# Optimization experiments

Measured on AMD Instinct MI355X. Metric: run time of the kernel, lower is better.

Reference implementation:

```python
import jax, jax.numpy as jnp
import numpy as np

B, S, D = 1, 2048, 2048
H, KVH, HD = 32, 8, 64
FFN = 8192
N_EXPERTS, TOP_K = 32, 4
EPS = 1e-5
NEG = -1e9


def setup_inputs() -> dict:
    key = jax.random.key(0)
    ks = jax.random.split(key, 24)
    s = 0.02
    inp = {}
    inp['hidden_states'] = jax.random.normal(ks[0], (B, S, D), jnp.float32)
    # RoPE tables: cos/sin of shape [B, S, HD]
    inv_freq = 1.0 / (10000.0 ** (np.arange(0, HD, 2, dtype=np.float32) / HD))
    t = np.arange(S, dtype=np.float32)
    freqs = np.outer(t, inv_freq)                      # [S, HD/2]
    emb = np.concatenate([freqs, freqs], axis=-1)      # [S, HD]
    inp['cos'] = jnp.asarray(np.cos(emb))[None].repeat(B, axis=0)
    inp['sin'] = jnp.asarray(np.sin(emb))[None].repeat(B, axis=0)
    # additive causal mask [B, 1, S, S]
    causal = jnp.where(jnp.tril(jnp.ones((S, S), bool)), 0.0, NEG).astype(jnp.float32)
    inp['attention_mask'] = jnp.broadcast_to(causal[None, None], (B, 1, S, S))
    # attention params
    inp['wq'] = jax.random.normal(ks[1], (H * HD, D), jnp.float32) * s
    inp['bq'] = jnp.zeros((H * HD,), jnp.float32)
    inp['wk'] = jax.random.normal(ks[2], (KVH * HD, D), jnp.float32) * s
    inp['bk'] = jnp.zeros((KVH * HD,), jnp.float32)
    inp['wv'] = jax.random.normal(ks[3], (KVH * HD, D), jnp.float32) * s
    inp['bv'] = jnp.zeros((KVH * HD,), jnp.float32)
    inp['wo'] = jax.random.normal(ks[4], (D, H * HD), jnp.float32) * s
    inp['bo'] = jnp.zeros((D,), jnp.float32)
    # norms
    inp['ln1_w'] = jnp.ones((D,), jnp.float32)
    inp['ln2_w'] = jnp.ones((D,), jnp.float32)
    # MoE gate + shared expert MLP
    inp['gate_w'] = jax.random.normal(ks[5], (N_EXPERTS, D), jnp.float32) * s
    inp['gate_b'] = jnp.zeros((N_EXPERTS,), jnp.float32)
    inp['w1'] = jax.random.normal(ks[6], (FFN, D), jnp.float32) * s
    inp['b1'] = jnp.zeros((FFN,), jnp.float32)
    inp['w2'] = jax.random.normal(ks[7], (D, FFN), jnp.float32) * s
    inp['b2'] = jnp.zeros((D,), jnp.float32)
    inp['w3'] = jax.random.normal(ks[8], (FFN, D), jnp.float32) * s
    inp['b3'] = jnp.zeros((FFN,), jnp.float32)
    return inp


def _rms_norm(x, w, eps=EPS):
    x32 = x.astype(jnp.float32)
    var = jnp.mean(x32 * x32, axis=-1, keepdims=True)
    return (w * (x32 * jax.lax.rsqrt(var + eps))).astype(x.dtype)


def _rotate_half(x):
    x1, x2 = jnp.split(x, 2, axis=-1)
    return jnp.concatenate([-x2, x1], axis=-1)


def _decoder_layer(hidden_states, cos, sin, attention_mask,
                   wq, bq, wk, bk, wv, bv, wo, bo, ln1_w, ln2_w,
                   gate_w, gate_b, w1, b1, w2, b2, w3, b3):
    residual = hidden_states
    x = _rms_norm(hidden_states, ln1_w)

    # projections -> [B, heads, S, HD]
    q = (x @ wq.T + bq).reshape(B, S, H, HD).transpose(0, 2, 1, 3)
    k = (x @ wk.T + bk).reshape(B, S, KVH, HD).transpose(0, 2, 1, 3)
    v = (x @ wv.T + bv).reshape(B, S, KVH, HD).transpose(0, 2, 1, 3)

    # RoPE (cos/sin unsqueezed on head dim)
    c, s_ = cos[:, None], sin[:, None]
    q = q * c + _rotate_half(q) * s_
    k = k * c + _rotate_half(k) * s_

    # GQA: repeat kv heads
    n_rep = H // KVH
    k = jnp.repeat(k, n_rep, axis=1)
    v = jnp.repeat(v, n_rep, axis=1)

    scaling = HD ** -0.5
    scores = jnp.einsum('bhqd,bhkd->bhqk', q, k) * scaling + attention_mask
    probs = jax.nn.softmax(scores.astype(jnp.float32), axis=-1).astype(q.dtype)
    attn = jnp.einsum('bhqk,bhkd->bhqd', probs, v)
    attn = attn.transpose(0, 2, 1, 3).reshape(B, S, H * HD)
    attn = attn @ wo.T + bo

    hidden_states = residual + attn
    residual = hidden_states
    x = _rms_norm(hidden_states, ln2_w)

    # MoE block (as written in source: router computed, but ALL tokens go
    # through one shared expert MLP; routing weights unused in output)
    flat = x.reshape(-1, D)
    router_logits = flat @ gate_w.T + gate_b                     # [B*S, E]
    rw = jax.nn.softmax(router_logits.astype(jnp.float32), axis=-1)
    rw_top, sel = jax.lax.top_k(rw, TOP_K)                       # computed, unused
    del rw_top, sel

    h1 = flat @ w1.T + b1
    h3 = flat @ w3.T + b3
    mlp = (jax.nn.silu(h1) * h3) @ w2.T + b2
    hidden_states = residual + mlp.reshape(B, S, D)
    return hidden_states


def reference(hidden_states, cos, sin, attention_mask,
              wq, bq, wk, bk, wv, bv, wo, bo, ln1_w, ln2_w,
              gate_w, gate_b, w1, b1, w2, b2, w3, b3):
    return _decoder_layer(hidden_states, cos, sin, attention_mask,
                          wq, bq, wk, bk, wv, bv, wo, bo, ln1_w, ln2_w,
                          gate_w, gate_b, w1, b1, w2, b2, w3, b3)
```

## Files before the change

kernel.cpp:

```cpp
#include <hip/hip_runtime.h>

#define S_LEN 2048
#define DMODEL 2048
#define NH 32
#define NKV 8
#define HD 64
#define FFN_DIM 8192

typedef __attribute__((ext_vector_type(4))) float f32x4;
typedef __attribute__((ext_vector_type(4))) unsigned u32x4;
typedef __attribute__((ext_vector_type(16))) float f32x16;
typedef __attribute__((ext_vector_type(8))) short bf16x8;

#define MFMA(a, b, c) __builtin_amdgcn_mfma_f32_16x16x32_bf16(a, b, c, 0, 0, 0)
#define MFMA32(a, b, c) __builtin_amdgcn_mfma_f32_32x32x16_bf16(a, b, c, 0, 0, 0)

__device__ __forceinline__ ushort f2bf(float f) {
  unsigned u = __float_as_uint(f);
  unsigned r = (u + 0x7fffu + ((u >> 16) & 1u)) >> 16;
  return (ushort)r;
}
__device__ __forceinline__ float bf2f(ushort s) {
  return __uint_as_float(((unsigned)s) << 16);
}
__device__ __forceinline__ unsigned cvtpk(float a, float b) {
  unsigned r;
  asm("v_cvt_pk_bf16_f32 %0, %1, %2" : "=v"(r) : "v"(a), "v"(b));
  return r;
}

__device__ __forceinline__ void gload16(const void* g, void* l) {
  __builtin_amdgcn_global_load_lds(
      (const __attribute__((address_space(1))) void*)g,
      (__attribute__((address_space(3))) void*)l, 16, 0, 0);
}

__device__ __forceinline__ bf16x8 dsr128(const ushort* p) {
  unsigned addr =
      (unsigned)(size_t)(const __attribute__((address_space(3))) ushort*)p;
  u32x4 r;
  asm volatile("ds_read_b128 %0, %1" : "=&v"(r) : "v"(addr));
  return __builtin_bit_cast(bf16x8, r);
}

__global__ __launch_bounds__(256) void cvt_k(const float* __restrict__ in,
                                             ushort* __restrict__ out) {
  int i = blockIdx.x * 256 + threadIdx.x;
  f32x4 a = ((const f32x4*)in)[i * 2];
  f32x4 b = ((const f32x4*)in)[i * 2 + 1];
  bf16x8 r;
#pragma unroll
  for (int j = 0; j < 4; j++) r[j] = (short)f2bf(a[j]);
#pragma unroll
  for (int j = 0; j < 4; j++) r[4 + j] = (short)f2bf(b[j]);
  ((bf16x8*)out)[i] = r;
}

__global__ __launch_bounds__(256) void cvt_qkv_k(const float* __restrict__ wq,
                                                 const float* __restrict__ wk,
                                                 const float* __restrict__ wv,
                                                 ushort* __restrict__ dst) {
  int row = blockIdx.x;
  const float* src;
  if (row < 2048) src = wq + (size_t)row * DMODEL;
  else if (row < 2560) src = wk + (size_t)(row - 2048) * DMODEL;
  else src = wv + (size_t)(row - 2560) * DMODEL;
  int i = threadIdx.x * 8;
  f32x4 a = *(const f32x4*)(src + i);
  f32x4 b = *(const f32x4*)(src + i + 4);
  bf16x8 r;
#pragma unroll
  for (int j = 0; j < 4; j++) r[j] = (short)f2bf(a[j]);
#pragma unroll
  for (int j = 0; j < 4; j++) r[4 + j] = (short)f2bf(b[j]);
  *(bf16x8*)(dst + (size_t)row * DMODEL + i) = r;
}

__global__ __launch_bounds__(256) void bias3_k(const float* __restrict__ a,
                                               const float* __restrict__ b,
                                               const float* __restrict__ c,
                                               float* __restrict__ out) {
  int i = blockIdx.x * 256 + threadIdx.x;
  float v;
  if (i < 2048) v = a[i];
  else if (i < 2560) v = b[i - 2048];
  else v = c[i - 2560];
  out[i] = v;
}

__global__ __launch_bounds__(256) void rmsnorm_k(const float* __restrict__ in,
                                                 const float* __restrict__ w,
                                                 ushort* __restrict__ out) {
  const int row = blockIdx.x;
  const int tid = threadIdx.x;
  const float* x = in + (size_t)row * DMODEL;
  f32x4 v0 = *(const f32x4*)(x + tid * 8);
  f32x4 v1 = *(const f32x4*)(x + tid * 8 + 4);
  float ss = v0[0] * v0[0] + v0[1] * v0[1] + v0[2] * v0[2] + v0[3] * v0[3] +
             v1[0] * v1[0] + v1[1] * v1[1] + v1[2] * v1[2] + v1[3] * v1[3];
#pragma unroll
  for (int off = 32; off; off >>= 1) ss += __shfl_xor(ss, off, 64);
  __shared__ float red[4];
  if ((tid & 63) == 0) red[tid >> 6] = ss;
  __syncthreads();
  float tot = red[0] + red[1] + red[2] + red[3];
  float inv = rsqrtf(tot * (1.f / DMODEL) + 1e-5f);
#pragma unroll
  for (int i = 0; i < 8; i++) {
    int c = tid * 8 + i;
    float val = (i < 4) ? v0[i] : v1[i - 4];
    out[(size_t)row * DMODEL + c] = f2bf(w[c] * val * inv);
  }
}

__global__ __launch_bounds__(256) void rope_k(ushort* __restrict__ qkv,
                                              const float* __restrict__ cs,
                                              const float* __restrict__ sn) {
  int idx = blockIdx.x * 256 + threadIdx.x;
  int d = idx & 31;
  int t = idx >> 5;
  int head = t % (NH + NKV);
  int s = t / (NH + NKV);
  int col = (head < NH) ? head * HD : DMODEL + (head - NH) * HD;
  ushort* p = qkv + (size_t)s * 3072 + col;
  float lo = bf2f(p[d]), hi = bf2f(p[d + 32]);
  float c = cs[s * HD + d], si = sn[s * HD + d];
  p[d] = f2bf(lo * c - hi * si);
  p[d + 32] = f2bf(hi * c + lo * si);
}

enum { EPI_BF16 = 0, EPI_RESID = 1, EPI_SILU = 2, EPI_MUL = 3, EPI_PART = 4 };

#define QUAD(AS, BS, MROW, NCOL)                                     \
  _Pragma("unroll") for (int kk_ = 0; kk_ < 2; kk_++)                \
  _Pragma("unroll") for (int mf_ = 0; mf_ < 4; mf_++)                \
  _Pragma("unroll") for (int nf_ = 0; nf_ < 2; nf_++)                \
      acc[(MROW) + mf_][(NCOL) + nf_] =                              \
          MFMA(AS[2 * mf_ + kk_], BS[2 * nf_ + kk_],                 \
               acc[(MROW) + mf_][(NCOL) + nf_]);

#define PHASE_MID                                    \
  __builtin_amdgcn_sched_barrier(0);                 \
  __builtin_amdgcn_s_barrier();                      \
  asm volatile("s_waitcnt lgkmcnt(0)" ::: "memory"); \
  __builtin_amdgcn_sched_barrier(0);                 \
  __builtin_amdgcn_s_setprio(1);

#define PHASE_CLOSE                                  \
  __builtin_amdgcn_s_setprio(0);                     \
  __builtin_amdgcn_sched_barrier(0);                 \
  __builtin_amdgcn_s_barrier();

#define RD_A(PA0, PA1, J0)                           \
  _Pragma("unroll") for (int j_ = 0; j_ < 4; j_++) { \
    A_[2 * j_] = dsr128((PA0) + ((J0) + j_) * 1024); \
    A_[2 * j_ + 1] = dsr128((PA1) + ((J0) + j_) * 1024); \
  }
#define RD_B(DST, PB0, PB1, J0)                      \
  _Pragma("unroll") for (int n_ = 0; n_ < 2; n_++) { \
    DST[2 * n_] = dsr128((PB0) + ((J0) + n_) * 1024);\
    DST[2 * n_ + 1] = dsr128((PB1) + ((J0) + n_) * 1024); \
  }

template <int EPI>
__global__ __launch_bounds__(512, 2) void gemm256(
    const ushort* __restrict__ A, int lda, const ushort* __restrict__ B,
    int ldb, const float* __restrict__ bias, const float* __restrict__ resid,
    ushort* __restrict__ outb, float* __restrict__ outf, int ldc, int K,
    int kspan, long long opart) {
  __shared__ __align__(16) ushort lds[65536];
  const int tid = threadIdx.x;
  const int l = tid & 63, w = tid >> 6;
  const int g = l >> 4, r16 = l & 15;
  const int wm = w >> 2, wn = w & 3;

  int nwg = gridDim.x * gridDim.y;
  int bid = blockIdx.y * gridDim.x + blockIdx.x;
  bid = (bid & 7) * (nwg >> 3) + (bid >> 3);
  const int m0 = (bid % gridDim.x) * 256;
  const int n0 = (bid / gridDim.x) * 256;
  const int z = blockIdx.z;

  const ushort* Ag = A + (size_t)z * kspan + (size_t)m0 * lda;
  const ushort* Bg = B + (size_t)z * kspan + (size_t)n0 * ldb;
  ushort* outbz = outb;
  if (EPI == EPI_PART) outbz = outb + (size_t)z * opart;

  const int NT = K >> 6, NI = NT >> 1;

  const int stgRow = w * 8 + (l >> 3);
  const int stgCol = ((l & 7) ^ (l >> 3)) * 8;

  const int xa = (r16 & 7) << 4;
  const int c0 = ((g * 16) ^ xa) >> 1;
  const int c1 = c0 ^ 32;
  const int aslot = wm ? 24576 : 8192;
  const int bslot = ((wn >> 1) ? 16384 : 0) + (wn & 1) * 4096;
  const ushort* pA0b0 = lds + aslot + r16 * 64 + c0;
  const ushort* pA1b0 = lds + aslot + r16 * 64 + c1;
  const ushort* pA0b1 = pA0b0 + 32768;
  const ushort* pA1b1 = pA1b0 + 32768;
  const ushort* pB0b0 = lds + bslot + r16 * 64 + c0;
  const ushort* pB1b0 = lds + bslot + r16 * 64 + c1;
  const ushort* pB0b1 = pB0b0 + 32768;
  const ushort* pB1b1 = pB1b0 + 32768;

  f32x4 acc[8][4];
#pragma unroll
  for (int i = 0; i < 8; i++)
#pragma unroll
    for (int j = 0; j < 4; j++) acc[i][j] = (f32x4){0, 0, 0, 0};

  auto stageA = [&](int slot, int tile, int hf) {
    ushort* dst = lds + ((tile & 1) * 32768 + slot * 8192 + w * 512);
    const ushort* src =
        Ag + (size_t)(hf * 128 + stgRow) * lda + tile * 64 + stgCol;
    gload16(src, dst);
    gload16(src + (size_t)64 * lda, dst + 4096);
  };
  auto stageB = [&](int slot, int tile, int hf) {
    ushort* dst = lds + ((tile & 1) * 32768 + slot * 8192 + w * 512);
    const ushort* src =
        Bg + (size_t)(hf * 128 + stgRow) * ldb + tile * 64 + stgCol;
    gload16(src, dst);
    gload16(src + (size_t)64 * ldb, dst + 4096);
  };

  stageB(0, 0, 0);
  stageB(2, 0, 1);
  stageA(1, 0, 0);
  stageA(3, 0, 1);
  stageB(0, 1, 0);
  stageB(2, 1, 1);
  asm volatile("s_waitcnt vmcnt(4)" ::: "memory");
  __builtin_amdgcn_s_barrier();

  bf16x8 A_[8], Blo[4], Bhi[4];

  for (int i = 0; i < NI; ++i) {
    const int ta = 2 * i, tb = 2 * i + 1;
    const bool st = (ta + 2 < NT);
    RD_A(pA0b0, pA1b0, 0);
    RD_B(Blo, pB0b0, pB1b0, 0);
    stageA(1, tb, 0);
    asm volatile("s_waitcnt lgkmcnt(8)" ::: "memory");
    PHASE_MID; QUAD(A_, Blo, 0, 0); PHASE_CLOSE;
    RD_B(Bhi, pB0b0, pB1b0, 2);
    stageA(3, tb, 1);
    PHASE_MID; QUAD(A_, Bhi, 0, 2); PHASE_CLOSE;
    RD_A(pA0b0, pA1b0, 4);
    if (st) stageB(0, ta + 2, 0);
    PHASE_MID; QUAD(A_, Bhi, 4, 2); PHASE_CLOSE;
    if (st) stageB(2, ta + 2, 1);
    PHASE_MID; QUAD(A_, Blo, 4, 0);
    __builtin_amdgcn_s_setprio(0);
    __builtin_amdgcn_sched_barrier(0);
    if (st) {
      asm volatile("s_waitcnt vmcnt(4)" ::: "memory");
    } else {
      asm volatile("s_waitcnt vmcnt(0)" ::: "memory");
    }
    __builtin_amdgcn_s_barrier();
    RD_A(pA0b1, pA1b1, 0);
    RD_B(Blo, pB0b1, pB1b1, 0);
    if (st) stageA(1, ta + 2, 0);
    asm volatile("s_waitcnt lgkmcnt(8)" ::: "memory");
    PHASE_MID; QUAD(A_, Blo, 0, 0); PHASE_CLOSE;
    RD_B(Bhi, pB0b1, pB1b1, 2);
    if (st) stageA(3, ta + 2, 1);
    PHASE_MID; QUAD(A_, Bhi, 0, 2); PHASE_CLOSE;
    RD_A(pA0b1, pA1b1, 4);
    if (st) stageB(0, tb + 2, 0);
    PHASE_MID; QUAD(A_, Bhi, 4, 2); PHASE_CLOSE;
    if (st) stageB(2, tb + 2, 1);
    PHASE_MID; QUAD(A_, Blo, 4, 0);
    __builtin_amdgcn_s_setprio(0);
    __builtin_amdgcn_sched_barrier(0);
    asm volatile("s_waitcnt vmcnt(4)" ::: "memory");
    __builtin_amdgcn_s_barrier();
  }

#pragma unroll
  for (int mf = 0; mf < 8; mf++) {
#pragma unroll
    for (int nf = 0; nf < 4; nf++) {
      const int n = n0 + wn * 64 + nf * 16 + r16;
      float bia = (EPI == EPI_PART) ? 0.f : bias[n];
#pragma unroll
      for (int reg = 0; reg < 4; reg++) {
        const int m = m0 + wm * 128 + mf * 16 + g * 4 + reg;
        float v = acc[mf][nf][reg] + bia;
        if constexpr (EPI == EPI_BF16) {
          outbz[(size_t)m * ldc + n] = f2bf(v);
        } else if constexpr (EPI == EPI_RESID) {
          outf[(size_t)m * ldc + n] = v + resid[(size_t)m * ldc + n];
        } else if constexpr (EPI == EPI_SILU) {
          float sv = v / (1.f + __expf(-v));
          outbz[(size_t)m * ldc + n] = f2bf(sv);
        } else if constexpr (EPI == EPI_MUL) {
          float hv = bf2f(outbz[(size_t)m * ldc + n]);
          outbz[(size_t)m * ldc + n] = f2bf(v * hv);
        } else {
          outbz[(size_t)m * ldc + n] = f2bf(v);
        }
      }
    }
  }
}

template <int MODE>
__global__ __launch_bounds__(256) void reduce2_k(
    const ushort* __restrict__ part, long long pstride, int nz,
    const float* __restrict__ bias, int ncol, const float* __restrict__ resid,
    float* __restrict__ outf, ushort* __restrict__ outb) {
  long long i = (long long)(blockIdx.x * 256 + threadIdx.x) * 8;
  int col = (int)(i % ncol);
  float s[8];
#pragma unroll
  for (int j = 0; j < 8; j++) s[j] = bias[col + j];
  for (int zz = 0; zz < nz; zz++) {
    bf16x8 v = *(const bf16x8*)(part + zz * pstride + i);
#pragma unroll
    for (int j = 0; j < 8; j++) s[j] += bf2f((ushort)v[j]);
  }
  if constexpr (MODE == 1) {
#pragma unroll
    for (int j = 0; j < 8; j++) outf[i + j] = s[j] + resid[i + j];
  } else {
    bf16x8 r;
#pragma unroll
    for (int j = 0; j < 8; j++) r[j] = (short)f2bf(s[j]);
    *(bf16x8*)(outb + i) = r;
  }
}

__global__ __launch_bounds__(256, 3) void flash2_k(const ushort* __restrict__ qkv,
                                                   ushort* __restrict__ att) {
  const int bid = blockIdx.x;
  const int head = (bid >> 4) & 31;
  const int rmap = bid & 15;
  const int qb = (bid & 256) ? (15 - rmap) : rmap;
  const int kvh = head >> 2;
  const int tid = threadIdx.x;
  const int w = tid >> 6, l = tid & 63;
  const int h = l >> 5, q31 = l & 31;
  const int qw = qb * 128 + w * 32;
  const int qrow = qw + q31;

  __shared__ __align__(16) ushort lds[2][8192];

  bf16x8 qreg[4];
  {
    const ushort* qp = qkv + (size_t)qrow * 3072 + head * HD;
#pragma unroll
    for (int s = 0; s < 4; s++)
      qreg[s] = *(const bf16x8*)(qp + s * 16 + h * 8);
  }

  f32x16 oacc[2];
#pragma unroll
  for (int i = 0; i < 16; i++) { oacc[0][i] = 0.f; oacc[1][i] = 0.f; }
  float mreg = -1e30f, lsum = 0.f;

  const int nt = 2 * qb + 2;

  const int skv = tid >> 2;
  const int sch = (tid & 3) * 2;
  const int vkv = tid & 63;
  const int vd0 = (tid >> 6) * 16;

  const ushort* kg_base = qkv + DMODEL + kvh * HD;

  bf16x8 krA, krB, vrA, vrB;
  auto loadTile = [&](int jb) {
    const ushort* kg = kg_base + (size_t)jb * 64 * 3072;
    krA = *(const bf16x8*)(kg + (size_t)skv * 3072 + sch * 8);
    krB = *(const bf16x8*)(kg + (size_t)skv * 3072 + sch * 8 + 8);
    const ushort* vg = kg + 512;
    vrA = *(const bf16x8*)(vg + (size_t)vkv * 3072 + vd0);
    vrB = *(const bf16x8*)(vg + (size_t)vkv * 3072 + vd0 + 8);
  };
  auto writeTile = [&](int b) {
    ushort* kb = lds[b];
    *(bf16x8*)(kb + skv * 64 + ((sch ^ (skv & 7)) * 8)) = krA;
    *(bf16x8*)(kb + skv * 64 + (((sch + 1) ^ (skv & 7)) * 8)) = krB;
    ushort* vb = lds[b] + 4096;
#pragma unroll
    for (int i = 0; i < 8; i++) {
      int d = vd0 + i;
      vb[d * 64 + (((vkv >> 3) ^ (d & 7)) * 8) + (vkv & 7)] = (ushort)vrA[i];
    }
#pragma unroll
    for (int i = 0; i < 8; i++) {
      int d = vd0 + 8 + i;
      vb[d * 64 + (((vkv >> 3) ^ (d & 7)) * 8) + (vkv & 7)] = (ushort)vrB[i];
    }
  };

  loadTile(0);
  for (int jb = 0; jb < nt; ++jb) {
    const int b = jb & 1;
    writeTile(b);
    __syncthreads();
    if (jb + 1 < nt) loadTile(jb + 1);

    if (jb * 64 <= qw + 31) {
      const ushort* Kb = lds[b];
      const ushort* Vb = lds[b] + 4096;

      f32x16 sacc[2];
#pragma unroll
      for (int i = 0; i < 16; i++) { sacc[0][i] = 0.f; sacc[1][i] = 0.f; }
#pragma unroll
      for (int c = 0; c < 2; c++) {
        const int kvr = c * 32 + q31;
        const ushort* kp = Kb + kvr * 64;
        const int kx = kvr & 7;
#pragma unroll
        for (int s = 0; s < 4; s++) {
          bf16x8 kf = *(const bf16x8*)(kp + ((2 * s + h) ^ kx) * 8);
          sacc[c] = MFMA32(kf, qreg[s], sacc[c]);
        }
      }

      const bool diag = (jb * 64 + 63 > qw);
      if (diag) {
#pragma unroll
        for (int c = 0; c < 2; c++)
#pragma unroll
          for (int rg = 0; rg < 16; rg++) {
            int kvg = jb * 64 + c * 32 + (rg & 3) + 8 * (rg >> 2) + 4 * h;
            if (kvg > qrow) sacc[c][rg] = -1e30f;
          }
      }
      float tmax = sacc[0][0];
#pragma unroll
      for (int rg = 1; rg < 16; rg++) tmax = fmaxf(tmax, sacc[0][rg]);
#pragma unroll
      for (int rg = 0; rg < 16; rg++) tmax = fmaxf(tmax, sacc[1][rg]);
      tmax = fmaxf(tmax, __shfl_xor(tmax, 32));
      const float mn = fmaxf(mreg, tmax);
      const float resc = __expf((mreg - mn) * 0.125f);
      mreg = mn;
      float rsum = 0.f;
#pragma unroll
      for (int c = 0; c < 2; c++)
#pragma unroll
        for (int rg = 0; rg < 16; rg++) {
          float pv = __expf((sacc[c][rg] - mn) * 0.125f);
          sacc[c][rg] = pv;
          rsum += pv;
        }
      rsum += __shfl_xor(rsum, 32);
      lsum = lsum * resc + rsum;
      oacc[0] *= resc;
      oacc[1] *= resc;

      unsigned pw_[2][4][2];
#pragma unroll
      for (int c = 0; c < 2; c++)
#pragma unroll
        for (int rr = 0; rr < 4; rr++) {
          pw_[c][rr][0] = cvtpk(sacc[c][4 * rr + 0], sacc[c][4 * rr + 1]);
          pw_[c][rr][1] = cvtpk(sacc[c][4 * rr + 2], sacc[c][4 * rr + 3]);
        }

#pragma unroll
      for (int s = 0; s < 4; s++) {
        const int c = s >> 1, base = (s & 1) * 2;
        unsigned k0 = h ? pw_[c][base + 1][0] : pw_[c][base][0];
        unsigned k1 = h ? pw_[c][base + 1][1] : pw_[c][base][1];
        unsigned s0 = h ? pw_[c][base][0] : pw_[c][base + 1][0];
        unsigned s1 = h ? pw_[c][base][1] : pw_[c][base + 1][1];
        unsigned t0 = __shfl_xor(s0, 32);
        unsigned t1 = __shfl_xor(s1, 32);
        union { unsigned u[4]; bf16x8 v; } pf;
        pf.u[0] = h ? t0 : k0;
        pf.u[1] = h ? t1 : k1;
        pf.u[2] = h ? k0 : t0;
        pf.u[3] = h ? k1 : t1;
#pragma unroll
        for (int dt = 0; dt < 2; dt++) {
          const int d = dt * 32 + q31;
          bf16x8 vf =
              *(const bf16x8*)(Vb + d * 64 + ((2 * s + h) ^ (d & 7)) * 8);
          oacc[dt] = MFMA32(vf, pf.v, oacc[dt]);
        }
      }
    }
  }

  const float inv = 1.f / lsum;
  ushort* op = att + (size_t)qrow * DMODEL + head * HD;
#pragma unroll
  for (int dt = 0; dt < 2; dt++)
#pragma unroll
    for (int rr = 0; rr < 4; rr++) {
      const int d0 = dt * 32 + 8 * rr + 4 * h;
      unsigned lo = cvtpk(oacc[dt][4 * rr + 0] * inv, oacc[dt][4 * rr + 1] * inv);
      unsigned hi = cvtpk(oacc[dt][4 * rr + 2] * inv, oacc[dt][4 * rr + 3] * inv);
      uint2 v2;
      v2.x = lo;
      v2.y = hi;
      *(uint2*)(op + d0) = v2;
    }
}

extern "C" void kernel_launch(void* const* d_in, const int* in_sizes, int n_in,
                              void* d_out, int out_size, void* d_ws,
                              size_t ws_size, hipStream_t stream) {
  (void)in_sizes; (void)n_in; (void)out_size; (void)ws_size;
  const float* hidden = (const float*)d_in[0];
  const float* cosb = (const float*)d_in[1];
  const float* sinb = (const float*)d_in[2];
  const float* wq = (const float*)d_in[4];
  const float* bq = (const float*)d_in[5];
  const float* wk = (const float*)d_in[6];
  const float* bk = (const float*)d_in[7];
  const float* wv = (const float*)d_in[8];
  const float* bv = (const float*)d_in[9];
  const float* wo = (const float*)d_in[10];
  const float* bo = (const float*)d_in[11];
  const float* ln1 = (const float*)d_in[12];
  const float* ln2 = (const float*)d_in[13];
  const float* w1 = (const float*)d_in[16];
  const float* b1 = (const float*)d_in[17];
  const float* w2 = (const float*)d_in[18];
  const float* b2 = (const float*)d_in[19];
  const float* w3 = (const float*)d_in[20];
  const float* b3 = (const float*)d_in[21];
  float* out = (float*)d_out;

  char* ws = (char*)d_ws;
  ushort* x1 = (ushort*)ws;   ws += (size_t)S_LEN * DMODEL * 2;
  ushort* qkv = (ushort*)ws;  ws += (size_t)S_LEN * 3072 * 2;
  ushort* att = (ushort*)ws;  ws += (size_t)S_LEN * DMODEL * 2;
  ushort* x2 = (ushort*)ws;   ws += (size_t)S_LEN * DMODEL * 2;
  ushort* hbuf = (ushort*)ws; ws += (size_t)S_LEN * FFN_DIM * 2;
  ushort* wbuf = (ushort*)ws; ws += (size_t)FFN_DIM * DMODEL * 2;
  float* bqkv = (float*)ws;   ws += 3072 * 4;

  ushort* partQ = att;
  ushort* partO = x2;
  ushort* partW = x1;

  rmsnorm_k<<<S_LEN, 256, 0, stream>>>(hidden, ln1, x1);

  cvt_qkv_k<<<3072, 256, 0, stream>>>(wq, wk, wv, wbuf);
  bias3_k<<<12, 256, 0, stream>>>(bq, bk, bv, bqkv);

  gemm256<EPI_PART><<<dim3(8, 12, 2), 512, 0, stream>>>(
      x1, DMODEL, wbuf, DMODEL, nullptr, nullptr, partQ, nullptr, 3072, 1024,
      1024, (long long)S_LEN * 3072);
  reduce2_k<0><<<(S_LEN * 3072) / 2048, 256, 0, stream>>>(
      partQ, (long long)S_LEN * 3072, 2, bqkv, 3072, nullptr, nullptr, qkv);

  rope_k<<<(S_LEN * (NH + NKV) * 32) / 256, 256, 0, stream>>>(qkv, cosb, sinb);

  flash2_k<<<512, 256, 0, stream>>>(qkv, att);

  cvt_k<<<(2048 * 2048) / 2048, 256, 0, stream>>>(wo, wbuf);
  gemm256<EPI_PART><<<dim3(8, 8, 4), 512, 0, stream>>>(
      att, DMODEL, wbuf, DMODEL, nullptr, nullptr, partO, nullptr, DMODEL, 512,
      512, (long long)S_LEN * DMODEL);
  reduce2_k<1><<<(S_LEN * DMODEL) / 2048, 256, 0, stream>>>(
      partO, (long long)S_LEN * DMODEL, 4, bo, DMODEL, hidden, out, nullptr);

  rmsnorm_k<<<S_LEN, 256, 0, stream>>>(out, ln2, x2);

  cvt_k<<<(FFN_DIM * 2048) / 2048, 256, 0, stream>>>(w1, wbuf);
  gemm256<EPI_SILU><<<dim3(8, 32), 512, 0, stream>>>(
      x2, DMODEL, wbuf, DMODEL, b1, nullptr, hbuf, nullptr, FFN_DIM, DMODEL, 0,
      0);

  cvt_k<<<(FFN_DIM * 2048) / 2048, 256, 0, stream>>>(w3, wbuf);
  gemm256<EPI_MUL><<<dim3(8, 32), 512, 0, stream>>>(
      x2, DMODEL, wbuf, DMODEL, b3, nullptr, hbuf, nullptr, FFN_DIM, DMODEL, 0,
      0);

  cvt_k<<<(DMODEL * FFN_DIM) / 2048, 256, 0, stream>>>(w2, wbuf);
  gemm256<EPI_PART><<<dim3(8, 8, 4), 512, 0, stream>>>(
      hbuf, FFN_DIM, wbuf, FFN_DIM, nullptr, nullptr, partW, nullptr, DMODEL,
      DMODEL, DMODEL, (long long)S_LEN * DMODEL);
  reduce2_k<1><<<(S_LEN * DMODEL) / 2048, 256, 0, stream>>>(
      partW, (long long)S_LEN * DMODEL, 4, b2, DMODEL, out, out, nullptr);
}
```

Baseline: 426.9 us.

## Fuse w1/w3 GEMMs with interleaved weights, fuse reductions with RoPE and RMSNorm

Converts w1 and w3 into one interleaved bf16 weight buffer so a single GEMM computes both projections and applies SiLU(h1)*h3 in its epilogue. This removes the second pass over x2 and the read-modify-write of hbuf. The partial-sum reductions are fused with RoPE for QKV and with the residual add plus RMSNorm after the output projection, which removes separate rope and rmsnorm kernels. It also swaps inline-asm ds_read_b128 for plain vector LDS loads, and doubles the weight workspace to hold the interleaved buffer.

Result: faster. 381.8 us (-10.6%).

```diff
diff --git a/kernel.cpp b/kernel.cpp
--- a/kernel.cpp
+++ b/kernel.cpp
@@ -8,7 +8,6 @@
 #define FFN_DIM 8192
 
 typedef __attribute__((ext_vector_type(4))) float f32x4;
-typedef __attribute__((ext_vector_type(4))) unsigned u32x4;
 typedef __attribute__((ext_vector_type(16))) float f32x16;
 typedef __attribute__((ext_vector_type(8))) short bf16x8;
 
@@ -33,14 +32,6 @@
   __builtin_amdgcn_global_load_lds(
       (const __attribute__((address_space(1))) void*)g,
       (__attribute__((address_space(3))) void*)l, 16, 0, 0);
-}
-
-__device__ __forceinline__ bf16x8 dsr128(const ushort* p) {
-  unsigned addr =
-      (unsigned)(size_t)(const __attribute__((address_space(3))) ushort*)p;
-  u32x4 r;
-  asm volatile("ds_read_b128 %0, %1" : "=&v"(r) : "v"(addr));
-  return __builtin_bit_cast(bf16x8, r);
 }
 
 __global__ __launch_bounds__(256) void cvt_k(const float* __restrict__ in,
@@ -76,6 +67,25 @@
   *(bf16x8*)(dst + (size_t)row * DMODEL + i) = r;
 }
 
+__global__ __launch_bounds__(256) void cvt_w13_k(const float* __restrict__ w1,
+                                                 const float* __restrict__ w3,
+                                                 ushort* __restrict__ dst) {
+  int r = blockIdx.x;
+  int nb = r >> 8, i5 = r & 255;
+  int wn = i5 >> 6, nf = (i5 >> 4) & 3, e = i5 & 15;
+  int L = nb * 128 + wn * 32 + (nf >> 1) * 16 + e;
+  const float* src = ((nf & 1) ? w3 : w1) + (size_t)L * DMODEL;
+  int i = threadIdx.x * 8;
+  f32x4 a = *(const f32x4*)(src + i);
+  f32x4 b = *(const f32x4*)(src + i + 4);
+  bf16x8 rr;
+#pragma unroll
+  for (int j = 0; j < 4; j++) rr[j] = (short)f2bf(a[j]);
+#pragma unroll
+  for (int j = 0; j < 4; j++) rr[4 + j] = (short)f2bf(b[j]);
+  *(bf16x8*)(dst + (size_t)r * DMODEL + i) = rr;
+}
+
 __global__ __launch_bounds__(256) void bias3_k(const float* __restrict__ a,
                                                const float* __restrict__ b,
                                                const float* __restrict__ c,
@@ -113,23 +123,7 @@
   }
 }
 
-__global__ __launch_bounds__(256) void rope_k(ushort* __restrict__ qkv,
-                                              const float* __restrict__ cs,
-                                              const float* __restrict__ sn) {
-  int idx = blockIdx.x * 256 + threadIdx.x;
-  int d = idx & 31;
-  int t = idx >> 5;
-  int head = t % (NH + NKV);
-  int s = t / (NH + NKV);
-  int col = (head < NH) ? head * HD : DMODEL + (head - NH) * HD;
-  ushort* p = qkv + (size_t)s * 3072 + col;
-  float lo = bf2f(p[d]), hi = bf2f(p[d + 32]);
-  float c = cs[s * HD + d], si = sn[s * HD + d];
-  p[d] = f2bf(lo * c - hi * si);
-  p[d + 32] = f2bf(hi * c + lo * si);
-}
-
-enum { EPI_BF16 = 0, EPI_RESID = 1, EPI_SILU = 2, EPI_MUL = 3, EPI_PART = 4 };
+enum { EPI_PART = 0, EPI_SILU2 = 1 };
 
 #define QUAD(AS, BS, MROW, NCOL)                                     \
   _Pragma("unroll") for (int kk_ = 0; kk_ < 2; kk_++)                \
@@ -153,21 +147,20 @@
 
 #define RD_A(PA0, PA1, J0)                           \
   _Pragma("unroll") for (int j_ = 0; j_ < 4; j_++) { \
-    A_[2 * j_] = dsr128((PA0) + ((J0) + j_) * 1024); \
-    A_[2 * j_ + 1] = dsr128((PA1) + ((J0) + j_) * 1024); \
+    A_[2 * j_] = *(const bf16x8*)((PA0) + ((J0) + j_) * 1024);     \
+    A_[2 * j_ + 1] = *(const bf16x8*)((PA1) + ((J0) + j_) * 1024); \
   }
 #define RD_B(DST, PB0, PB1, J0)                      \
   _Pragma("unroll") for (int n_ = 0; n_ < 2; n_++) { \
-    DST[2 * n_] = dsr128((PB0) + ((J0) + n_) * 1024);\
-    DST[2 * n_ + 1] = dsr128((PB1) + ((J0) + n_) * 1024); \
+    DST[2 * n_] = *(const bf16x8*)((PB0) + ((J0) + n_) * 1024);     \
+    DST[2 * n_ + 1] = *(const bf16x8*)((PB1) + ((J0) + n_) * 1024); \
   }
 
 template <int EPI>
 __global__ __launch_bounds__(512, 2) void gemm256(
     const ushort* __restrict__ A, int lda, const ushort* __restrict__ B,
-    int ldb, const float* __restrict__ bias, const float* __restrict__ resid,
-    ushort* __restrict__ outb, float* __restrict__ outf, int ldc, int K,
-    int kspan, long long opart) {
+    int ldb, const float* __restrict__ b1v, const float* __restrict__ b3v,
+    ushort* __restrict__ outb, int ldc, int K, int kspan, long long opart) {
   __shared__ __align__(16) ushort lds[65536];
   const int tid = threadIdx.x;
   const int l = tid & 63, w = tid >> 6;
@@ -183,8 +176,7 @@
 
   const ushort* Ag = A + (size_t)z * kspan + (size_t)m0 * lda;
   const ushort* Bg = B + (size_t)z * kspan + (size_t)n0 * ldb;
-  ushort* outbz = outb;
-  if (EPI == EPI_PART) outbz = outb + (size_t)z * opart;
+  ushort* outbz = outb + (size_t)z * opart;
 
   const int NT = K >> 6, NI = NT >> 1;
 
@@ -280,58 +272,131 @@
     __builtin_amdgcn_s_barrier();
   }
 
-#pragma unroll
-  for (int mf = 0; mf < 8; mf++) {
-#pragma unroll
-    for (int nf = 0; nf < 4; nf++) {
-      const int n = n0 + wn * 64 + nf * 16 + r16;
-      float bia = (EPI == EPI_PART) ? 0.f : bias[n];
-#pragma unroll
-      for (int reg = 0; reg < 4; reg++) {
-        const int m = m0 + wm * 128 + mf * 16 + g * 4 + reg;
-        float v = acc[mf][nf][reg] + bia;
-        if constexpr (EPI == EPI_BF16) {
-          outbz[(size_t)m * ldc + n] = f2bf(v);
-        } else if constexpr (EPI == EPI_RESID) {
-          outf[(size_t)m * ldc + n] = v + resid[(size_t)m * ldc + n];
-        } else if constexpr (EPI == EPI_SILU) {
-          float sv = v / (1.f + __expf(-v));
-          outbz[(size_t)m * ldc + n] = f2bf(sv);
-        } else if constexpr (EPI == EPI_MUL) {
-          float hv = bf2f(outbz[(size_t)m * ldc + n]);
-          outbz[(size_t)m * ldc + n] = f2bf(v * hv);
-        } else {
-          outbz[(size_t)m * ldc + n] = f2bf(v);
+  if constexpr (EPI == EPI_PART) {
+#pragma unroll
+    for (int mf = 0; mf < 8; mf++)
+#pragma unroll
+      for (int nf = 0; nf < 4; nf++) {
+        const int n = n0 + wn * 64 + nf * 16 + r16;
+#pragma unroll
+        for (int reg = 0; reg < 4; reg++) {
+          const int m = m0 + wm * 128 + mf * 16 + g * 4 + reg;
+          outbz[(size_t)m * ldc + n] = f2bf(acc[mf][nf][reg]);
         }
       }
-    }
-  }
-}
-
-template <int MODE>
-__global__ __launch_bounds__(256) void reduce2_k(
-    const ushort* __restrict__ part, long long pstride, int nz,
-    const float* __restrict__ bias, int ncol, const float* __restrict__ resid,
-    float* __restrict__ outf, ushort* __restrict__ outb) {
+  } else {
+#pragma unroll
+    for (int mf = 0; mf < 8; mf++)
+#pragma unroll
+      for (int p = 0; p < 2; p++) {
+        const int L = (n0 >> 1) + wn * 32 + p * 16 + r16;
+        const float bb1 = b1v[L], bb3 = b3v[L];
+#pragma unroll
+        for (int reg = 0; reg < 4; reg++) {
+          const int m = m0 + wm * 128 + mf * 16 + g * 4 + reg;
+          float h1 = acc[mf][2 * p][reg] + bb1;
+          float h3 = acc[mf][2 * p + 1][reg] + bb3;
+          float sv = h1 / (1.f + __expf(-h1));
+          outbz[(size_t)m * ldc + L] = f2bf(sv * h3);
+        }
+      }
+  }
+}
+
+__global__ __launch_bounds__(384) void reduceQ_rope_k(
+    const ushort* __restrict__ part, const float* __restrict__ bias,
+    const float* __restrict__ cs, const float* __restrict__ sn,
+    ushort* __restrict__ qkv) {
+  __shared__ float row[3072];
+  const int r = blockIdx.x;
+  const int col = threadIdx.x * 8;
+  const long long ps = (long long)S_LEN * 3072;
+  float s[8];
+#pragma unroll
+  for (int j = 0; j < 8; j++) s[j] = bias[col + j];
+#pragma unroll
+  for (int z = 0; z < 2; z++) {
+    bf16x8 v = *(const bf16x8*)(part + z * ps + (size_t)r * 3072 + col);
+#pragma unroll
+    for (int j = 0; j < 8; j++) s[j] += bf2f((ushort)v[j]);
+  }
+#pragma unroll
+  for (int j = 0; j < 8; j++) row[col + j] = s[j];
+  __syncthreads();
+  ushort o[8];
+  if (col < 2560) {
+    const float* c = cs + r * HD + (col & 63);
+    const float* si = sn + r * HD + (col & 63);
+    const float sgn = (col & 32) ? 1.f : -1.f;
+    const int pc = col ^ 32;
+#pragma unroll
+    for (int j = 0; j < 8; j++)
+      o[j] = f2bf(s[j] * c[j] + sgn * row[pc + j] * si[j]);
+  } else {
+#pragma unroll
+    for (int j = 0; j < 8; j++) o[j] = f2bf(s[j]);
+  }
+  bf16x8 rr;
+#pragma unroll
+  for (int j = 0; j < 8; j++) rr[j] = (short)o[j];
+  *(bf16x8*)(qkv + (size_t)r * 3072 + col) = rr;
+}
+
+__global__ __launch_bounds__(256) void reduceO_rms_k(
+    const ushort* __restrict__ part, const float* __restrict__ bias,
+    const float* __restrict__ resid, const float* __restrict__ lnw,
+    float* __restrict__ outf, ushort* __restrict__ x2) {
+  const int r = blockIdx.x;
+  const int tid = threadIdx.x;
+  const int col = tid * 8;
+  const long long ps = (long long)S_LEN * DMODEL;
+  float s[8];
+#pragma unroll
+  for (int j = 0; j < 8; j++) s[j] = bias[col + j] + resid[(size_t)r * DMODEL + col + j];
+#pragma unroll
+  for (int z = 0; z < 4; z++) {
+    bf16x8 v = *(const bf16x8*)(part + z * ps + (size_t)r * DMODEL + col);
+#pragma unroll
+    for (int j = 0; j < 8; j++) s[j] += bf2f((ushort)v[j]);
+  }
+  float ss = 0.f;
+#pragma unroll
+  for (int j = 0; j < 8; j++) ss += s[j] * s[j];
+#pragma unroll
+  for (int off = 32; off; off >>= 1) ss += __shfl_xor(ss, off, 64);
+  __shared__ float red[4];
+  if ((tid & 63) == 0) red[tid >> 6] = ss;
+  f32x4 o0, o1;
+#pragma unroll
+  for (int j = 0; j < 4; j++) { o0[j] = s[j]; o1[j] = s[4 + j]; }
+  *(f32x4*)(outf + (size_t)r * DMODEL + col) = o0;
+  *(f32x4*)(outf + (size_t)r * DMODEL + col + 4) = o1;
+  __syncthreads();
+  float tot = red[0] + red[1] + red[2] + red[3];
+  float inv = rsqrtf(tot * (1.f / DMODEL) + 1e-5f);
+  bf16x8 rr;
+#pragma unroll
+  for (int j = 0; j < 8; j++) rr[j] = (short)f2bf(lnw[col + j] * s[j] * inv);
+  *(bf16x8*)(x2 + (size_t)r * DMODEL + col) = rr;
+}
+
+__global__ __launch_bounds__(256) void reduceW_k(
+    const ushort* __restrict__ part, const float* __restrict__ bias,
+    float* __restrict__ out) {
   long long i = (long long)(blockIdx.x * 256 + threadIdx.x) * 8;
-  int col = (int)(i % ncol);
+  int col = (int)(i % DMODEL);
+  const long long ps = (long long)S_LEN * DMODEL;
   float s[8];
 #pragma unroll
-  for (int j = 0; j < 8; j++) s[j] = bias[col + j];
-  for (int zz = 0; zz < nz; zz++) {
-    bf16x8 v = *(const bf16x8*)(part + zz * pstride + i);
+  for (int j = 0; j < 8; j++) s[j] = bias[col + j] + out[i + j];
+#pragma unroll
+  for (int z = 0; z < 4; z++) {
+    bf16x8 v = *(const bf16x8*)(part + z * ps + i);
 #pragma unroll
     for (int j = 0; j < 8; j++) s[j] += bf2f((ushort)v[j]);
   }
-  if constexpr (MODE == 1) {
-#pragma unroll
-    for (int j = 0; j < 8; j++) outf[i + j] = s[j] + resid[i + j];
-  } else {
-    bf16x8 r;
-#pragma unroll
-    for (int j = 0; j < 8; j++) r[j] = (short)f2bf(s[j]);
-    *(bf16x8*)(outb + i) = r;
-  }
+#pragma unroll
+  for (int j = 0; j < 8; j++) out[i + j] = s[j];
 }
 
 __global__ __launch_bounds__(256, 3) void flash2_k(const ushort* __restrict__ qkv,
@@ -537,11 +602,11 @@
   ushort* att = (ushort*)ws;  ws += (size_t)S_LEN * DMODEL * 2;
   ushort* x2 = (ushort*)ws;   ws += (size_t)S_LEN * DMODEL * 2;
   ushort* hbuf = (ushort*)ws; ws += (size_t)S_LEN * FFN_DIM * 2;
-  ushort* wbuf = (ushort*)ws; ws += (size_t)FFN_DIM * DMODEL * 2;
+  ushort* wbuf = (ushort*)ws; ws += (size_t)2 * FFN_DIM * DMODEL * 2;
   float* bqkv = (float*)ws;   ws += 3072 * 4;
 
   ushort* partQ = att;
-  ushort* partO = x2;
+  ushort* partO = hbuf;
   ushort* partW = x1;
 
   rmsnorm_k<<<S_LEN, 256, 0, stream>>>(hidden, ln1, x1);
@@ -550,38 +615,25 @@
   bias3_k<<<12, 256, 0, stream>>>(bq, bk, bv, bqkv);
 
   gemm256<EPI_PART><<<dim3(8, 12, 2), 512, 0, stream>>>(
-      x1, DMODEL, wbuf, DMODEL, nullptr, nullptr, partQ, nullptr, 3072, 1024,
-      1024, (long long)S_LEN * 3072);
-  reduce2_k<0><<<(S_LEN * 3072) / 2048, 256, 0, stream>>>(
-      partQ, (long long)S_LEN * 3072, 2, bqkv, 3072, nullptr, nullptr, qkv);
-
-  rope_k<<<(S_LEN * (NH + NKV) * 32) / 256, 256, 0, stream>>>(qkv, cosb, sinb);
+      x1, DMODEL, wbuf, DMODEL, nullptr, nullptr, partQ, 3072, 1024, 1024,
+      (long long)S_LEN * 3072);
+  reduceQ_rope_k<<<S_LEN, 384, 0, stream>>>(partQ, bqkv, cosb, sinb, qkv);
 
   flash2_k<<<512, 256, 0, stream>>>(qkv, att);
 
   cvt_k<<<(2048 * 2048) / 2048, 256, 0, stream>>>(wo, wbuf);
   gemm256<EPI_PART><<<dim3(8, 8, 4), 512, 0, stream>>>(
-      att, DMODEL, wbuf, DMODEL, nullptr, nullptr, partO, nullptr, DMODEL, 512,
-      512, (long long)S_LEN * DMODEL);
-  reduce2_k<1><<<(S_LEN * DMODEL) / 2048, 256, 0, stream>>>(
-      partO, (long long)S_LEN * DMODEL, 4, bo, DMODEL, hidden, out, nullptr);
-
-  rmsnorm_k<<<S_LEN, 256, 0, stream>>>(out, ln2, x2);
-
-  cvt_k<<<(FFN_DIM * 2048) / 2048, 256, 0, stream>>>(w1, wbuf);
-  gemm256<EPI_SILU><<<dim3(8, 32), 512, 0, stream>>>(
-      x2, DMODEL, wbuf, DMODEL, b1, nullptr, hbuf, nullptr, FFN_DIM, DMODEL, 0,
-      0);
-
-  cvt_k<<<(FFN_DIM * 2048) / 2048, 256, 0, stream>>>(w3, wbuf);
-  gemm256<EPI_MUL><<<dim3(8, 32), 512, 0, stream>>>(
-      x2, DMODEL, wbuf, DMODEL, b3, nullptr, hbuf, nullptr, FFN_DIM, DMODEL, 0,
-      0);
+      att, DMODEL, wbuf, DMODEL, nullptr, nullptr, partO, DMODEL, 512, 512,
+      (long long)S_LEN * DMODEL);
+  reduceO_rms_k<<<S_LEN, 256, 0, stream>>>(partO, bo, hidden, ln2, out, x2);
+
+  cvt_w13_k<<<2 * FFN_DIM, 256, 0, stream>>>(w1, w3, wbuf);
+  gemm256<EPI_SILU2><<<dim3(8, 64), 512, 0, stream>>>(
+      x2, DMODEL, wbuf, DMODEL, b1, b3, hbuf, FFN_DIM, DMODEL, 0, 0);
 
   cvt_k<<<(DMODEL * FFN_DIM) / 2048, 256, 0, stream>>>(w2, wbuf);
   gemm256<EPI_PART><<<dim3(8, 8, 4), 512, 0, stream>>>(
-      hbuf, FFN_DIM, wbuf, FFN_DIM, nullptr, nullptr, partW, nullptr, DMODEL,
-      DMODEL, DMODEL, (long long)S_LEN * DMODEL);
-  reduce2_k<1><<<(S_LEN * DMODEL) / 2048, 256, 0, stream>>>(
-      partW, (long long)S_LEN * DMODEL, 4, b2, DMODEL, out, out, nullptr);
-}
+      hbuf, FFN_DIM, wbuf, FFN_DIM, nullptr, nullptr, partW, DMODEL, 2048,
+      2048, (long long)S_LEN * DMODEL);
+  reduceW_k<<<(S_LEN * DMODEL) / 2048, 256, 0, stream>>>(partW, b2, out);
+}
```
